# Kernel tuning notes

Hardware: AMD Instinct MI355X
Metric: run time of the kernel (lower is better)

Reference implementation:

```python
import jax, jax.numpy as jnp
import numpy as np
import math

D_MODEL = 1024
EXPAND = 2
D_INNER = D_MODEL * EXPAND  # 2048
D_STATE = 16
DT_RANK = max(1, (D_MODEL + 15) // 16)  # 64
K = 4  # conv kernel size
B, S = 2, 2048


def silu(v):
    return v * jax.nn.sigmoid(v)


def setup_inputs() -> dict:
    key = jax.random.key(0)
    ks = jax.random.split(key, 12)
    sc = lambda fan_in: 1.0 / math.sqrt(fan_in)
    x = jax.random.normal(ks[0], (B, S, D_MODEL), dtype=jnp.float32)
    Win = jax.random.normal(ks[1], (D_MODEL, 2 * D_INNER), dtype=jnp.float32) * sc(D_MODEL)
    Wconv = jax.random.normal(ks[2], (D_INNER, 1, K), dtype=jnp.float32) * sc(K)
    bconv = jax.random.normal(ks[3], (D_INNER,), dtype=jnp.float32) * 0.01
    Wx = jax.random.normal(ks[4], (D_INNER, DT_RANK + 2 * D_STATE), dtype=jnp.float32) * sc(D_INNER)
    Wdt = jax.random.normal(ks[5], (DT_RANK, D_INNER), dtype=jnp.float32) * sc(DT_RANK)
    # dt_proj bias init: inverse-softplus of dt ~ LogUniform[1e-3, 1e-1]
    dt = jnp.exp(jax.random.uniform(ks[6], (D_INNER,)) * (math.log(0.1) - math.log(0.001)) + math.log(0.001))
    dt = jnp.clip(dt, 0.0001, None)
    bdt = dt + jnp.log(-jnp.expm1(-dt))
    a = jnp.arange(1, D_STATE + 1, dtype=jnp.float32)[None, :].repeat(D_INNER, axis=0)
    a = a + jax.random.uniform(ks[7], a.shape) * 0.1
    A_log = jnp.log(a)
    Dp = jnp.ones((D_INNER,), dtype=jnp.float32)
    Wout = jax.random.normal(ks[8], (D_INNER, D_MODEL), dtype=jnp.float32) * sc(D_INNER)
    return {"x": x, "Win": Win, "Wconv": Wconv, "bconv": bconv, "Wx": Wx,
            "Wdt": Wdt, "bdt": bdt, "A_log": A_log, "Dp": Dp, "Wout": Wout}


def causal_dw_conv(x, Wconv, bconv):
    # x: [B, S, C] -> depthwise causal conv along S
    xc = jnp.transpose(x, (0, 2, 1))  # [B, C, S]
    y = jax.lax.conv_general_dilated(
        xc, Wconv, window_strides=(1,), padding=[(K - 1, 0)],
        feature_group_count=D_INNER,
        dimension_numbers=("NCH", "OIH", "NCH"))
    y = y + bconv[None, :, None]
    return jnp.transpose(y, (0, 2, 1))  # [B, S, C]


def selective_scan(u, delta, b_term, c_term, A_log, Dp):
    # u, delta: [B,S,Di]; b_term, c_term: [B,S,Ds]
    a = -jnp.exp(A_log)  # [Di, Ds]
    delta_a = jnp.exp(delta[..., None] * a[None, None])            # [B,S,Di,Ds] fp32
    delta_b_u = (delta * u)[..., None] * b_term[:, :, None, :]     # [B,S,Di,Ds]
    du = u * Dp[None, None, :]                                     # [B,S,Di]
    # time-major for scan
    dA = jnp.transpose(delta_a, (1, 0, 2, 3))
    dBu = jnp.transpose(delta_b_u, (1, 0, 2, 3))
    c_t = jnp.transpose(c_term, (1, 0, 2))
    du_t = jnp.transpose(du, (1, 0, 2))

    def step(state, inp):
        dA_t, dBu_t, c, duv = inp
        state = dA_t * state + dBu_t                  # [B,Di,Ds]
        y = jnp.einsum("bdn,bn->bd", state, c) + duv  # [B,Di]
        return state, y

    init = jnp.zeros((u.shape[0], D_INNER, D_STATE), dtype=jnp.float32)
    _, ys = jax.lax.scan(step, init, (dA, dBu, c_t, du_t))
    return jnp.transpose(ys, (1, 0, 2))  # [B,S,Di]


def reference(x, Win, Wconv, bconv, Wx, Wdt, bdt, A_log, Dp, Wout):
    xz = x @ Win                              # [B,S,2*Di]
    x_branch, z_branch = jnp.split(xz, 2, axis=-1)
    x_branch = silu(causal_dw_conv(x_branch, Wconv, bconv))
    params = x_branch @ Wx                    # [B,S,R+2*Ds]
    delta, b_term, c_term = jnp.split(params, [DT_RANK, DT_RANK + D_STATE], axis=-1)
    delta = jax.nn.softplus(delta @ Wdt + bdt)
    y = selective_scan(x_branch, delta, b_term, c_term, A_log, Dp)
    y = y * silu(z_branch)
    return y @ Wout
```

## Files before the change

kernel.cpp:

```cpp
#include <hip/hip_runtime.h>

typedef unsigned short u16;
typedef _Float16 f16;
typedef f16 f16x8 __attribute__((ext_vector_type(8)));
typedef u16 u16x8 __attribute__((ext_vector_type(8)));
typedef short s16x8 __attribute__((ext_vector_type(8)));
typedef float f32x4 __attribute__((ext_vector_type(4)));
typedef float f32x8 __attribute__((ext_vector_type(8)));

#define T_TOK 4096
#define B_SZ 2
#define S_LEN 2048
#define DMODEL 1024
#define DI 2048
#define DS 16
#define RNK 64
#define NCH 64
#define CLEN 32
#define LDXZ 4096
#define SK 8
#define PRM_SLICE (4096 * 128)
#define LOG2E 1.4426950408889634f

#define GLOAD_LDS16(gp, lp)                                                                   \
  __builtin_amdgcn_global_load_lds((const __attribute__((address_space(1))) void*)(gp),       \
                                   (__attribute__((address_space(3))) void*)(lp), 16, 0, 0)

__device__ __forceinline__ float b2f(u16 v) { return __uint_as_float(((unsigned)v) << 16); }
__device__ __forceinline__ u16 f2b(float f) {
  unsigned u = __float_as_uint(f);
  return (u16)((u + 0x7fffu + ((u >> 16) & 1u)) >> 16);
}
__device__ __forceinline__ float fexp2(float x) {
#if __has_builtin(__builtin_amdgcn_exp2f)
  return __builtin_amdgcn_exp2f(x);
#else
  return exp2f(x);
#endif
}
__device__ __forceinline__ int dtype_of(const void* dp) {
  unsigned v = *(const unsigned*)dp;
  return (v == 0x3F800000u) ? 0 : (v == 0x3C003C00u) ? 2 : 1;
}
__device__ __forceinline__ float load_any(const void* p, size_t i, int flag) {
  if (flag == 0) return ((const float*)p)[i];
  if (flag == 1) return b2f(((const u16*)p)[i]);
  return (float)((const f16*)p)[i];
}

__device__ __forceinline__ void tr_tile(const void* __restrict__ src, void* __restrict__ dst,
                                        int R, int C, int Cpad, int f, int bx, int by, int ob) {
  __shared__ f16 t[32][33];
  int c0 = bx * 32, r0 = by * 32;
  int tx = threadIdx.x & 31, ty = threadIdx.x >> 5;
#pragma unroll
  for (int i = ty; i < 32; i += 8) {
    int r = r0 + i, c = c0 + tx;
    float v = (r < R && c < C) ? load_any(src, (size_t)r * C + c, f) : 0.f;
    t[i][tx] = (f16)v;
  }
  __syncthreads();
#pragma unroll
  for (int i = ty; i < 32; i += 8) {
    int c = c0 + i, r = r0 + tx;
    if (c < Cpad && r < R) {
      if (ob) ((u16*)dst)[(size_t)c * R + r] = f2b((float)t[tx][i]);
      else ((f16*)dst)[(size_t)c * R + r] = t[tx][i];
    }
  }
}

__global__ __launch_bounds__(256) void k_prep(const void* __restrict__ Wconv, const void* __restrict__ bconv,
                                              const void* __restrict__ bdt, const void* __restrict__ A_log,
                                              const void* __restrict__ Dp, const void* __restrict__ Wx,
                                              const void* __restrict__ Wdt, const void* __restrict__ Win,
                                              const void* __restrict__ x, f16* __restrict__ WxT,
                                              f16* __restrict__ WdtT, u16* __restrict__ WinTb,
                                              u16* __restrict__ xhb, float* __restrict__ a_f,
                                              float* __restrict__ wconv_f, float* __restrict__ bconv_f,
                                              float* __restrict__ bdt_f, float* __restrict__ dp_f,
                                              int* __restrict__ flag) {
  int f = dtype_of(Dp);
  int bid = blockIdx.x, t = threadIdx.x;
  if (bid < 128) {
    int i = bid * 256 + t;
    a_f[i] = -__expf(load_any(A_log, i, f)) * LOG2E;
  } else if (bid < 160) {
    int i = (bid - 128) * 256 + t;
    wconv_f[i] = load_any(Wconv, i, f);
  } else if (bid < 168) {
    int i = (bid - 160) * 256 + t;
    bconv_f[i] = load_any(bconv, i, f);
  } else if (bid < 176) {
    int i = (bid - 168) * 256 + t;
    bdt_f[i] = load_any(bdt, i, f);
  } else if (bid < 184) {
    int i = (bid - 176) * 256 + t;
    dp_f[i] = load_any(Dp, i, f);
  } else if (bid == 184) {
    if (t == 0) *flag = f;
  } else if (bid < 441) {
    int id = bid - 185;
    tr_tile(Wx, WxT, 2048, 96, 128, f, id & 3, id >> 2, 0);
  } else if (bid < 569) {
    int id = bid - 441;
    tr_tile(Wdt, WdtT, 64, 2048, 2048, f, id & 63, id >> 6, 0);
  } else if (bid < 4665) {
    int id = bid - 569;
    tr_tile(Win, WinTb, 1024, 4096, 4096, f, id & 127, id >> 7, 1);
  } else {
    if (f == 1) return;
    size_t i = (size_t)(bid - 4665) * 2048 + (size_t)t * 8;
    u16x8 o;
    if (f == 0) {
      const float* s = (const float*)x + i;
#pragma unroll
      for (int j = 0; j < 8; ++j) o[j] = f2b(s[j]);
    } else {
      const f16* s = (const f16*)x + i;
#pragma unroll
      for (int j = 0; j < 8; ++j) o[j] = f2b((float)s[j]);
    }
    *(u16x8*)(xhb + i) = o;
  }
}

__global__ __launch_bounds__(256) void k_transpose16(const void* __restrict__ src, f16* __restrict__ dst,
                                                     int R, int C, int Cpad, const void* __restrict__ Dp) {
  tr_tile(src, dst, R, C, Cpad, dtype_of(Dp), blockIdx.x, blockIdx.y, 0);
}

__global__ __launch_bounds__(512) void k_gemm1(const void* __restrict__ x0, const u16* __restrict__ xhb,
                                               const u16* __restrict__ Bw, f16* __restrict__ C,
                                               const int* __restrict__ flag) {
  constexpr int LD = 1024, LDC = LDXZ, NT = 16, NP = NT / 2;
  __shared__ __align__(16) u16 lds[8 * 8192];
  const u16* A = (*flag == 1) ? (const u16*)x0 : xhb;
  const int tid = threadIdx.x;
  const int wv = tid >> 6, ln = tid & 63;
  const int quad = ln >> 4, l16 = ln & 15;
  const int wr = wv >> 2, wc = wv & 3;
  const int m0 = blockIdx.y * 256, n0 = blockIdx.x * 256;
  const int rr = tid >> 3;
  const int cc = (tid & 7) ^ (rr & 7);
  const u16* aBase = A + (size_t)m0 * LD + cc * 8;
  const u16* bBase = Bw + (size_t)n0 * LD + cc * 8;
  const int brow = ((tid >> 8) << 6) + (rr & 31);
  u16* const dBase = lds + wv * 512;
  auto stageA = [&](int tile, int mq) {
    const u16* s = aBase + (size_t)(mq * 64 + rr) * LD + tile * 64;
    u16* d = dBase + ((tile & 1) * 4 + mq) * 8192;
    GLOAD_LDS16(s, d);
    GLOAD_LDS16(s + 128 * LD, d + 4096);
  };
  auto stageB = [&](int tile, int nq) {
    const u16* s = bBase + (size_t)(brow + nq * 32) * LD + tile * 64;
    u16* d = dBase + ((tile & 1) * 4 + 2 + nq) * 8192;
    GLOAD_LDS16(s, d);
    GLOAD_LDS16(s + 128 * LD, d + 4096);
  };
  const int rxor = (l16 & 7) << 3;
  f32x4 acc[8][4] = {};
  stageA(0, 0); stageB(0, 1); stageB(0, 0); stageA(0, 1);
  stageA(1, 0); stageB(1, 1);
  asm volatile("s_waitcnt vmcnt(4)" ::: "memory");
  __builtin_amdgcn_s_barrier();
  s16x8 af[4][2], bf[2][2];
  for (int pr = 0; pr < NP; ++pr) {
    const int t0 = 2 * pr;
    const bool more = (pr < NP - 1);
#pragma unroll
    for (int ph = 0; ph < 8; ++ph) {
      const int slot = ph >> 2, q = ph & 3;
      const int mq = q >> 1, nq = (q >> 1) ^ (q & 1);
      const u16* Ar = lds + (slot * 4 + mq) * 8192;
      const u16* Br = lds + (slot * 4 + 2 + nq) * 8192;
      if (q == 0 || q == 2) {
#pragma unroll
        for (int i = 0; i < 4; ++i) {
          const int ra = wr * 64 + i * 16 + l16;
#pragma unroll
          for (int kk = 0; kk < 2; ++kk)
            af[i][kk] = *(const s16x8*)(Ar + ra * 64 + ((kk * 32 + quad * 8) ^ rxor));
        }
      }
      if (q != 2) {
#pragma unroll
        for (int j = 0; j < 2; ++j) {
          const int rb = wc * 32 + j * 16 + l16;
#pragma unroll
          for (int kk = 0; kk < 2; ++kk)
            bf[j][kk] = *(const s16x8*)(Br + rb * 64 + ((kk * 32 + quad * 8) ^ rxor));
        }
      }
      if (ph == 0) stageB(t0 + 1, 0);
      else if (ph == 1) stageA(t0 + 1, 1);
      else if (more) {
        if (ph == 2) stageA(t0 + 2, 0);
        else if (ph == 3) stageB(t0 + 2, 1);
        else if (ph == 4) stageB(t0 + 2, 0);
        else if (ph == 5) stageA(t0 + 2, 1);
        else if (ph == 6) stageA(t0 + 3, 0);
        else stageB(t0 + 3, 1);
      }
      __builtin_amdgcn_s_barrier();
      asm volatile("s_waitcnt lgkmcnt(0)" ::: "memory");
      __builtin_amdgcn_sched_barrier(0);
      __builtin_amdgcn_s_setprio(1);
#pragma unroll
      for (int kk = 0; kk < 2; ++kk)
#pragma unroll
        for (int i = 0; i < 4; ++i)
#pragma unroll
          for (int j = 0; j < 2; ++j)
            acc[mq * 4 + i][nq * 2 + j] = __builtin_amdgcn_mfma_f32_16x16x32_bf16(
                af[i][kk], bf[j][kk], acc[mq * 4 + i][nq * 2 + j], 0, 0, 0);
      __builtin_amdgcn_s_setprio(0);
      if (ph == 3) {
        if (more) asm volatile("s_waitcnt vmcnt(6)" ::: "memory");
        else asm volatile("s_waitcnt vmcnt(2)" ::: "memory");
      } else if (ph == 5) {
        if (more) asm volatile("s_waitcnt vmcnt(8)" ::: "memory");
        else asm volatile("s_waitcnt vmcnt(0)" ::: "memory");
      } else if (ph == 7) {
        if (more) asm volatile("s_waitcnt vmcnt(4)" ::: "memory");
        else asm volatile("s_waitcnt vmcnt(0)" ::: "memory");
      }
      __builtin_amdgcn_s_barrier();
    }
  }
#pragma unroll
  for (int i = 0; i < 8; ++i)
#pragma unroll
    for (int j = 0; j < 4; ++j)
#pragma unroll
      for (int r = 0; r < 4; ++r) {
        const int row = m0 + wr * 128 + i * 16 + quad * 4 + r;
        const int col = n0 + wc * 64 + j * 16 + l16;
        C[(size_t)row * LDC + col] = (f16)acc[i][j][r];
      }
}

template <int BM, int BN, int EPI>
__global__ __launch_bounds__(256) void k_gemm2(const f16* __restrict__ A, const f16* __restrict__ B,
                                               void* __restrict__ Cv, const float* __restrict__ bias,
                                               const int* __restrict__ flag,
                                               int klen, int lda, int ldb, int ldc) {
  constexpr int WM = BM / 2, WN = BN / 2;
  constexpr int FM = WM / 16, FN = WN / 16;
  __shared__ __align__(16) f16 As[2 * BM * 32];
  __shared__ __align__(16) f16 Bs[2 * BN * 32];
  const int tid = threadIdx.x;
  const int wv = tid >> 6, ln = tid & 63;
  const int quad = ln >> 4, l16 = ln & 15;
  const int lrow = ln >> 2, lch = (ln & 3) * 8;
  const int m0 = blockIdx.y * BM, n0 = blockIdx.x * BN;
  const int wm = (wv & 1) * WM, wn = (wv >> 1) * WN;
  const int kbase = blockIdx.z * klen;
  f32x4 acc[FM][FN] = {};
  for (int kk = 0; kk < klen; kk += 64) {
    const int k0 = kbase + kk;
    __syncthreads();
#pragma unroll
    for (int h = 0; h < 2; ++h) {
#pragma unroll
      for (int i = 0; i < BM / 64; ++i) {
        int r0 = wv * (BM / 4) + i * 16;
        GLOAD_LDS16(A + (size_t)(m0 + r0 + lrow) * lda + k0 + h * 32 + lch, As + h * BM * 32 + r0 * 32);
      }
#pragma unroll
      for (int i = 0; i < BN / 64; ++i) {
        int r0 = wv * (BN / 4) + i * 16;
        GLOAD_LDS16(B + (size_t)(n0 + r0 + lrow) * ldb + k0 + h * 32 + lch, Bs + h * BN * 32 + r0 * 32);
      }
    }
    __syncthreads();
#pragma unroll
    for (int h = 0; h < 2; ++h) {
      f16x8 af[FM], bf[FN];
#pragma unroll
      for (int i = 0; i < FM; ++i) af[i] = *(const f16x8*)(As + h * BM * 32 + (wm + i * 16 + l16) * 32 + quad * 8);
#pragma unroll
      for (int j = 0; j < FN; ++j) bf[j] = *(const f16x8*)(Bs + h * BN * 32 + (wn + j * 16 + l16) * 32 + quad * 8);
#pragma unroll
      for (int i = 0; i < FM; ++i)
#pragma unroll
        for (int j = 0; j < FN; ++j)
          acc[i][j] = __builtin_amdgcn_mfma_f32_16x16x32_f16(af[i], bf[j], acc[i][j], 0, 0, 0);
    }
  }
  int dflag = 1;
  if constexpr (EPI == 2) dflag = *flag;
  f16* Cz = (f16*)Cv;
  if constexpr (EPI == 4) Cz = (f16*)Cv + (size_t)blockIdx.z * PRM_SLICE;
#pragma unroll
  for (int i = 0; i < FM; ++i)
#pragma unroll
    for (int j = 0; j < FN; ++j)
#pragma unroll
      for (int r = 0; r < 4; ++r) {
        int row = m0 + wm + i * 16 + quad * 4 + r;
        int col = n0 + wn + j * 16 + l16;
        size_t ci = (size_t)row * ldc + col;
        float v = acc[i][j][r];
        if constexpr (EPI == 1) {
          v += bias[col];
          v = (v > 20.f) ? v : log1pf(__expf(v));
          Cz[ci] = (f16)v;
        } else if constexpr (EPI == 2) {
          if (dflag == 0) ((float*)Cv)[ci] = v;
          else if (dflag == 1) ((u16*)Cv)[ci] = f2b(v);
          else ((f16*)Cv)[ci] = (f16)v;
        } else {
          Cz[ci] = (f16)v;
        }
      }
}

__global__ __launch_bounds__(256) void k_sum_prm(const f16* __restrict__ parts, f16* __restrict__ prm,
                                                 float* __restrict__ prmBC) {
  size_t i = (size_t)(blockIdx.x * 256 + threadIdx.x) * 8;
  int col0 = (int)(i & 127);
  if (col0 >= 96) return;
  float s[8] = {};
#pragma unroll
  for (int z = 0; z < SK; ++z) {
    f16x8 v = *(const f16x8*)(parts + (size_t)z * PRM_SLICE + i);
#pragma unroll
    for (int j = 0; j < 8; ++j) s[j] += (float)v[j];
  }
  if (col0 < 64) {
    f16x8 o;
#pragma unroll
    for (int j = 0; j < 8; ++j) o[j] = (f16)s[j];
    *(f16x8*)(prm + i) = o;
  } else {
    size_t tok = i >> 7;
    f32x8 of;
#pragma unroll
    for (int j = 0; j < 8; ++j) of[j] = s[j];
    *(f32x8*)(prmBC + tok * 32 + (col0 - 64)) = of;
  }
}

__global__ __launch_bounds__(256) void k_conv_silu(const f16* __restrict__ xz, const float* __restrict__ Wconv,
                                                   const float* __restrict__ bconv, f16* __restrict__ xc) {
  int t = blockIdx.x;
  int s = t & (S_LEN - 1);
  int d8 = threadIdx.x * 8;
  float w[4][8];
#pragma unroll
  for (int i = 0; i < 8; ++i)
#pragma unroll
    for (int j = 0; j < 4; ++j) w[j][i] = Wconv[(d8 + i) * 4 + j];
  float acc[8];
#pragma unroll
  for (int i = 0; i < 8; ++i) acc[i] = bconv[d8 + i];
#pragma unroll
  for (int j = 0; j < 4; ++j) {
    int sl = s - 3 + j;
    if (sl >= 0) {
      f16x8 xv = *(const f16x8*)(xz + (size_t)(t - 3 + j) * LDXZ + d8);
#pragma unroll
      for (int i = 0; i < 8; ++i) acc[i] = fmaf((float)xv[i], w[j][i], acc[i]);
    }
  }
  f16x8 o;
#pragma unroll
  for (int i = 0; i < 8; ++i) {
    float v = acc[i];
    o[i] = (f16)(v / (1.f + __expf(-v)));
  }
  *(f16x8*)(xc + (size_t)t * DI + d8) = o;
}

__global__ __launch_bounds__(256) void k_scan_passA(const f16* __restrict__ dlt, const f16* __restrict__ u,
                                                    const float* __restrict__ prmBC, const float* __restrict__ a_f,
                                                    f16* __restrict__ lcs, float* __restrict__ sumdv) {
  int g = blockIdx.x * 256 + threadIdx.x;
  int nh = g & 1, p = g >> 1;
  int d = p & (DI - 1);
  int c = (p >> 11) & (NCH - 1);
  int b = p >> 17;
  f32x4 a0 = *(const f32x4*)(a_f + d * DS + nh * 8);
  f32x4 a1 = *(const f32x4*)(a_f + d * DS + nh * 8 + 4);
  float a[8] = {a0[0], a0[1], a0[2], a0[3], a1[0], a1[1], a1[2], a1[3]};
  float st[8] = {};
  float sumd = 0.f;
  int t0 = b * S_LEN + c * CLEN;
  const f16* dp = dlt + (size_t)t0 * LDXZ + d;
  const f16* up = u + (size_t)t0 * DI + d;
  const float* bp = prmBC + (size_t)t0 * 32 + nh * 8;
  float dl = (float)dp[0];
  float uv = (float)up[0];
  for (int s = 0; s < CLEN; ++s) {
    int sn = (s + 1 < CLEN) ? s + 1 : s;
    float dl_n = (float)dp[(size_t)sn * LDXZ];
    float uv_n = (float)up[(size_t)sn * DI];
    f32x8 bv = *(const f32x8*)(bp + (size_t)s * 32);
    sumd += dl;
    float dbu = dl * uv;
#pragma unroll
    for (int j = 0; j < 8; ++j) {
      float e = fexp2(dl * a[j]);
      st[j] = fmaf(e, st[j], dbu * bv[j]);
    }
    dl = dl_n;
    uv = uv_n;
  }
  f16x8 o;
#pragma unroll
  for (int j = 0; j < 8; ++j) o[j] = (f16)st[j];
  *(f16x8*)(lcs + (size_t)p * DS + nh * 8) = o;
  if (nh == 0) sumdv[p] = sumd;
}

__global__ __launch_bounds__(256) void k_scan_passB(f16* __restrict__ lcs, const float* __restrict__ sumdv,
                                                    const float* __restrict__ a_f) {
  int g = blockIdx.x * 256 + threadIdx.x;
  int n = g & 15, d = (g >> 4) & (DI - 1), b = g >> 15;
  float an = a_f[d * DS + n];
  float init = 0.f;
  for (int c = 0; c < NCH; ++c) {
    int p = (b * NCH + c) * DI + d;
    size_t idx = (size_t)p * DS + n;
    float l = (float)lcs[idx];
    lcs[idx] = (f16)init;
    init = fexp2(sumdv[p] * an) * init + l;
  }
}

__global__ __launch_bounds__(256) void k_scan_passC(const f16* __restrict__ dlt, const f16* __restrict__ u,
                                                    const float* __restrict__ prmBC, const float* __restrict__ a_f,
                                                    const float* __restrict__ dp_f, const f16* __restrict__ lcs,
                                                    f16* __restrict__ xz) {
  int g = blockIdx.x * 256 + threadIdx.x;
  int nh = g & 1, p = g >> 1;
  int d = p & (DI - 1);
  int c = (p >> 11) & (NCH - 1);
  int b = p >> 17;
  f32x4 a0 = *(const f32x4*)(a_f + d * DS + nh * 8);
  f32x4 a1 = *(const f32x4*)(a_f + d * DS + nh * 8 + 4);
  float a[8] = {a0[0], a0[1], a0[2], a0[3], a1[0], a1[1], a1[2], a1[3]};
  float st[8];
  f16x8 iv = *(const f16x8*)(lcs + (size_t)p * DS + nh * 8);
#pragma unroll
  for (int j = 0; j < 8; ++j) st[j] = (float)iv[j];
  float dpv = dp_f[d];
  int t0 = b * S_LEN + c * CLEN;
  const f16* dp = dlt + (size_t)t0 * LDXZ + d;
  const f16* up = u + (size_t)t0 * DI + d;
  const float* bp = prmBC + (size_t)t0 * 32 + nh * 8;
  f16* zp = xz + (size_t)t0 * LDXZ + DI + d;
  float dl = (float)dp[0];
  float uv = (float)up[0];
  float z = (float)zp[0];
  for (int s = 0; s < CLEN; ++s) {
    int sn = (s + 1 < CLEN) ? s + 1 : s;
    float dl_n = (float)dp[(size_t)sn * LDXZ];
    float uv_n = (float)up[(size_t)sn * DI];
    float z_n = (float)zp[(size_t)sn * LDXZ];
    f32x8 bv = *(const f32x8*)(bp + (size_t)s * 32);
    f32x8 cv = *(const f32x8*)(bp + (size_t)s * 32 + 16);
    float dbu = dl * uv;
    float part = (nh == 0) ? uv * dpv : 0.f;
#pragma unroll
    for (int j = 0; j < 8; ++j) {
      float e = fexp2(dl * a[j]);
      st[j] = fmaf(e, st[j], dbu * bv[j]);
      part = fmaf(st[j], cv[j], part);
    }
    part += __shfl_xor(part, 1, 64);
    if (nh == 0) {
      float sg = 1.f / (1.f + __expf(-z));
      zp[(size_t)s * LDXZ] = (f16)(part * z * sg);
    }
    dl = dl_n;
    uv = uv_n;
    z = z_n;
  }
}

extern "C" void kernel_launch(void* const* d_in, const int* in_sizes, int n_in,
                              void* d_out, int out_size, void* d_ws, size_t ws_size,
                              hipStream_t stream) {
  const void* x = d_in[0];
  const void* Win = d_in[1];
  const void* Wconv = d_in[2];
  const void* bconv = d_in[3];
  const void* Wx = d_in[4];
  const void* Wdt = d_in[5];
  const void* bdt = d_in[6];
  const void* A_log = d_in[7];
  const void* Dp = d_in[8];
  const void* Wout = d_in[9];
  (void)in_sizes; (void)n_in; (void)out_size; (void)ws_size;

  const size_t KB = 1024, MB = 1024 * 1024;
  char* ws = (char*)d_ws;
  f16* xzh = (f16*)ws;
  u16* xhb = (u16*)(ws + 32 * MB);
  f16* xch = (f16*)(ws + 32 * MB);
  u16* WinTb = (u16*)(ws + 48 * MB);
  f16* parts = (f16*)(ws + 48 * MB);
  f16* lcs = (f16*)(ws + 48 * MB);
  f16* WoutT = (f16*)(ws + 48 * MB);
  float* sumd = (float*)(ws + 56 * MB);
  f16* prm = (f16*)(ws + 57 * MB);
  float* prmBC = (float*)(ws + 58 * MB);
  f16* WxT = (f16*)(ws + 58 * MB + 512 * KB);
  f16* WdtT = (f16*)(ws + 59 * MB);
  float* a_f = (float*)(ws + 59 * MB + 256 * KB);
  float* wconv_f = (float*)(ws + 59 * MB + 384 * KB);
  float* bconv_f = (float*)(ws + 59 * MB + 416 * KB);
  float* bdt_f = (float*)(ws + 59 * MB + 424 * KB);
  float* dp_f = (float*)(ws + 59 * MB + 432 * KB);
  int* flag = (int*)(ws + 59 * MB + 440 * KB);

  k_prep<<<6713, 256, 0, stream>>>(Wconv, bconv, bdt, A_log, Dp, Wx, Wdt, Win, x,
                                   WxT, WdtT, WinTb, xhb, a_f, wconv_f, bconv_f, bdt_f, dp_f, flag);

  k_gemm1<<<dim3(16, 16), 512, 0, stream>>>(x, xhb, WinTb, xzh, flag);
  k_conv_silu<<<T_TOK, 256, 0, stream>>>(xzh, wconv_f, bconv_f, xch);
  k_gemm2<64, 128, 4><<<dim3(1, 4096 / 64, SK), 256, 0, stream>>>(
      xch, WxT, parts, nullptr, flag, 2048 / SK, 2048, 2048, 128);
  k_sum_prm<<<PRM_SLICE / 8 / 256, 256, 0, stream>>>(parts, prm, prmBC);
  k_gemm2<128, 128, 1><<<dim3(2048 / 128, 4096 / 128), 256, 0, stream>>>(
      prm, WdtT, xzh, bdt_f, flag, 64, 128, 64, LDXZ);
  k_scan_passA<<<(B_SZ * NCH * DI * 2) / 256, 256, 0, stream>>>(xzh, xch, prmBC, a_f, lcs, sumd);
  k_scan_passB<<<(B_SZ * DI * DS) / 256, 256, 0, stream>>>(lcs, sumd, a_f);
  k_scan_passC<<<(B_SZ * NCH * DI * 2) / 256, 256, 0, stream>>>(xzh, xch, prmBC, a_f, dp_f, lcs, xzh);
  k_transpose16<<<dim3(1024 / 32, 2048 / 32), 256, 0, stream>>>(Wout, WoutT, 2048, 1024, 1024, Dp);
  k_gemm2<64, 128, 2><<<dim3(1024 / 128, 4096 / 64), 256, 0, stream>>>(
      xzh + DI, WoutT, d_out, nullptr, flag, 2048, LDXZ, 2048, 1024);
}
```

Baseline: 334.3 us.

## Store delta transposed per channel and software-pipeline scan pass loads

The delta projection GEMM now computes the transposed product (Wdt^T times params^T), so softplus(delta) is written channel-major into the xz buffer's delta region. The scan passes can then load each chunk's 32 delta values as four contiguous 8-wide vectors instead of 32 strided scalar loads. PassA, passB and passC also fully unroll their loops and prefetch u, z, B and C several steps ahead in register ring buffers to hide memory latency. The cost is more register pressure and reliance on the GEMM operand swap and new indexing being correct.

```diff
diff --git a/kernel.cpp b/kernel.cpp
--- a/kernel.cpp
+++ b/kernel.cpp
@@ -303,10 +303,11 @@
         int col = n0 + wn + j * 16 + l16;
         size_t ci = (size_t)row * ldc + col;
         float v = acc[i][j][r];
-        if constexpr (EPI == 1) {
-          v += bias[col];
+        if constexpr (EPI == 3) {
+          v += bias[row];
           v = (v > 20.f) ? v : log1pf(__expf(v));
-          Cz[ci] = (f16)v;
+          size_t di2 = ((size_t)(row << 1) + (col >> 11)) * (size_t)LDXZ + (col & 2047);
+          Cz[di2] = (f16)v;
         } else if constexpr (EPI == 2) {
           if (dflag == 0) ((float*)Cv)[ci] = v;
           else if (dflag == 1) ((u16*)Cv)[ci] = f2b(v);
@@ -374,7 +375,7 @@
   *(f16x8*)(xc + (size_t)t * DI + d8) = o;
 }
 
-__global__ __launch_bounds__(256) void k_scan_passA(const f16* __restrict__ dlt, const f16* __restrict__ u,
+__global__ __launch_bounds__(256) void k_scan_passA(const f16* __restrict__ dltT, const f16* __restrict__ u,
                                                     const float* __restrict__ prmBC, const float* __restrict__ a_f,
                                                     f16* __restrict__ lcs, float* __restrict__ sumdv) {
   int g = blockIdx.x * 256 + threadIdx.x;
@@ -385,19 +386,28 @@
   f32x4 a0 = *(const f32x4*)(a_f + d * DS + nh * 8);
   f32x4 a1 = *(const f32x4*)(a_f + d * DS + nh * 8 + 4);
   float a[8] = {a0[0], a0[1], a0[2], a0[3], a1[0], a1[1], a1[2], a1[3]};
+  int t0 = b * S_LEN + c * CLEN;
+  const f16* dp = dltT + (size_t)(2 * d + b) * LDXZ + c * CLEN;
+  const f16* up = u + (size_t)t0 * DI + d;
+  const float* bp = prmBC + (size_t)t0 * 32 + nh * 8;
+  f16x8 dlv[4];
+#pragma unroll
+  for (int q = 0; q < 4; ++q) dlv[q] = *(const f16x8*)(dp + q * 8);
+  float uf[4];
+#pragma unroll
+  for (int q = 0; q < 4; ++q) uf[q] = (float)up[(size_t)q * DI];
+  f32x8 bvv[2];
+#pragma unroll
+  for (int q = 0; q < 2; ++q) bvv[q] = *(const f32x8*)(bp + q * 32);
   float st[8] = {};
   float sumd = 0.f;
-  int t0 = b * S_LEN + c * CLEN;
-  const f16* dp = dlt + (size_t)t0 * LDXZ + d;
-  const f16* up = u + (size_t)t0 * DI + d;
-  const float* bp = prmBC + (size_t)t0 * 32 + nh * 8;
-  float dl = (float)dp[0];
-  float uv = (float)up[0];
+#pragma unroll
   for (int s = 0; s < CLEN; ++s) {
-    int sn = (s + 1 < CLEN) ? s + 1 : s;
-    float dl_n = (float)dp[(size_t)sn * LDXZ];
-    float uv_n = (float)up[(size_t)sn * DI];
-    f32x8 bv = *(const f32x8*)(bp + (size_t)s * 32);
+    float dl = (float)dlv[s >> 3][s & 7];
+    float uv = uf[s & 3];
+    f32x8 bv = bvv[s & 1];
+    if (s + 4 < CLEN) uf[s & 3] = (float)up[(size_t)(s + 4) * DI];
+    if (s + 2 < CLEN) bvv[s & 1] = *(const f32x8*)(bp + (s + 2) * 32);
     sumd += dl;
     float dbu = dl * uv;
 #pragma unroll
@@ -405,8 +415,6 @@
       float e = fexp2(dl * a[j]);
       st[j] = fmaf(e, st[j], dbu * bv[j]);
     }
-    dl = dl_n;
-    uv = uv_n;
   }
   f16x8 o;
 #pragma unroll
@@ -420,17 +428,30 @@
   int g = blockIdx.x * 256 + threadIdx.x;
   int n = g & 15, d = (g >> 4) & (DI - 1), b = g >> 15;
   float an = a_f[d * DS + n];
+  const size_t base = (size_t)b * NCH * DI + d;
+  float lf[4], sf[4];
+#pragma unroll
+  for (int q = 0; q < 4; ++q) {
+    size_t pq = base + (size_t)q * DI;
+    lf[q] = (float)lcs[pq * DS + n];
+    sf[q] = sumdv[pq];
+  }
   float init = 0.f;
+#pragma unroll
   for (int c = 0; c < NCH; ++c) {
-    int p = (b * NCH + c) * DI + d;
-    size_t idx = (size_t)p * DS + n;
-    float l = (float)lcs[idx];
-    lcs[idx] = (f16)init;
-    init = fexp2(sumdv[p] * an) * init + l;
-  }
-}
-
-__global__ __launch_bounds__(256) void k_scan_passC(const f16* __restrict__ dlt, const f16* __restrict__ u,
+    size_t pc = base + (size_t)c * DI;
+    float l = lf[c & 3], sd = sf[c & 3];
+    if (c + 4 < NCH) {
+      size_t pn = base + (size_t)(c + 4) * DI;
+      lf[c & 3] = (float)lcs[pn * DS + n];
+      sf[c & 3] = sumdv[pn];
+    }
+    lcs[pc * DS + n] = (f16)init;
+    init = fexp2(sd * an) * init + l;
+  }
+}
+
+__global__ __launch_bounds__(256) void k_scan_passC(const f16* __restrict__ dltT, const f16* __restrict__ u,
                                                     const float* __restrict__ prmBC, const float* __restrict__ a_f,
                                                     const float* __restrict__ dp_f, const f16* __restrict__ lcs,
                                                     f16* __restrict__ xz) {
@@ -448,20 +469,40 @@
   for (int j = 0; j < 8; ++j) st[j] = (float)iv[j];
   float dpv = dp_f[d];
   int t0 = b * S_LEN + c * CLEN;
-  const f16* dp = dlt + (size_t)t0 * LDXZ + d;
+  const f16* dp = dltT + (size_t)(2 * d + b) * LDXZ + c * CLEN;
   const f16* up = u + (size_t)t0 * DI + d;
   const float* bp = prmBC + (size_t)t0 * 32 + nh * 8;
   f16* zp = xz + (size_t)t0 * LDXZ + DI + d;
-  float dl = (float)dp[0];
-  float uv = (float)up[0];
-  float z = (float)zp[0];
+  f16x8 dlv[4];
+#pragma unroll
+  for (int q = 0; q < 4; ++q) dlv[q] = *(const f16x8*)(dp + q * 8);
+  float uf[4], zf[4];
+#pragma unroll
+  for (int q = 0; q < 4; ++q) {
+    uf[q] = (float)up[(size_t)q * DI];
+    zf[q] = (float)zp[(size_t)q * LDXZ];
+  }
+  f32x8 bvv[2], cvv[2];
+#pragma unroll
+  for (int q = 0; q < 2; ++q) {
+    bvv[q] = *(const f32x8*)(bp + q * 32);
+    cvv[q] = *(const f32x8*)(bp + q * 32 + 16);
+  }
+#pragma unroll
   for (int s = 0; s < CLEN; ++s) {
-    int sn = (s + 1 < CLEN) ? s + 1 : s;
-    float dl_n = (float)dp[(size_t)sn * LDXZ];
-    float uv_n = (float)up[(size_t)sn * DI];
-    float z_n = (float)zp[(size_t)sn * LDXZ];
-    f32x8 bv = *(const f32x8*)(bp + (size_t)s * 32);
-    f32x8 cv = *(const f32x8*)(bp + (size_t)s * 32 + 16);
+    float dl = (float)dlv[s >> 3][s & 7];
+    float uv = uf[s & 3];
+    float z = zf[s & 3];
+    f32x8 bv = bvv[s & 1];
+    f32x8 cv = cvv[s & 1];
+    if (s + 4 < CLEN) {
+      uf[s & 3] = (float)up[(size_t)(s + 4) * DI];
+      zf[s & 3] = (float)zp[(size_t)(s + 4) * LDXZ];
+    }
+    if (s + 2 < CLEN) {
+      bvv[s & 1] = *(const f32x8*)(bp + (s + 2) * 32);
+      cvv[s & 1] = *(const f32x8*)(bp + (s + 2) * 32 + 16);
+    }
     float dbu = dl * uv;
     float part = (nh == 0) ? uv * dpv : 0.f;
 #pragma unroll
@@ -475,9 +516,6 @@
       float sg = 1.f / (1.f + __expf(-z));
       zp[(size_t)s * LDXZ] = (f16)(part * z * sg);
     }
-    dl = dl_n;
-    uv = uv_n;
-    z = z_n;
   }
 }
 
@@ -525,8 +563,8 @@
   k_gemm2<64, 128, 4><<<dim3(1, 4096 / 64, SK), 256, 0, stream>>>(
       xch, WxT, parts, nullptr, flag, 2048 / SK, 2048, 2048, 128);
   k_sum_prm<<<PRM_SLICE / 8 / 256, 256, 0, stream>>>(parts, prm, prmBC);
-  k_gemm2<128, 128, 1><<<dim3(2048 / 128, 4096 / 128), 256, 0, stream>>>(
-      prm, WdtT, xzh, bdt_f, flag, 64, 128, 64, LDXZ);
+  k_gemm2<128, 128, 3><<<dim3(4096 / 128, 2048 / 128), 256, 0, stream>>>(
+      WdtT, prm, xzh, bdt_f, flag, 64, 64, 128, 0);
   k_scan_passA<<<(B_SZ * NCH * DI * 2) / 256, 256, 0, stream>>>(xzh, xch, prmBC, a_f, lcs, sumd);
   k_scan_passB<<<(B_SZ * DI * DS) / 256, 256, 0, stream>>>(lcs, sumd, a_f);
   k_scan_passC<<<(B_SZ * NCH * DI * 2) / 256, 256, 0, stream>>>(xzh, xch, prmBC, a_f, dp_f, lcs, xzh);
```

Result: slower. 343.3 us (+2.7%).
